# Optimization experiments

Hardware: AMD Instinct MI355X
Metric: run time of the kernel (lower is better)

The kernel has to match this reference:

```python
import jax, jax.numpy as jnp
import numpy as np
import math

B, T, C = 8, 1024, 64  # n_head = 1 (forced by the module's relative-attention matmul shapes)


def setup_inputs() -> dict:
    key = jax.random.key(0)
    ks = jax.random.split(key, 7)
    x = jax.random.normal(ks[0], (B, T, C), dtype=jnp.float32)
    Wqkv = jax.random.normal(ks[1], (3 * C, C), dtype=jnp.float32) * 0.02
    bqkv = jnp.zeros((3 * C,), dtype=jnp.float32)
    embk = jax.random.normal(ks[2], (T, C), dtype=jnp.float32) * 0.02
    embv = jax.random.normal(ks[3], (T, C), dtype=jnp.float32) * 0.02
    Wproj = jax.random.normal(ks[4], (C, C), dtype=jnp.float32) * 0.02
    bproj = jnp.zeros((C,), dtype=jnp.float32)
    return {"x": x, "Wqkv": Wqkv, "bqkv": bqkv, "embk": embk, "embv": embv,
            "Wproj": Wproj, "bproj": bproj}


def reference(x, Wqkv, bqkv, embk, embv, Wproj, bproj):
    b, t, c = x.shape
    qkv = x @ Wqkv.T + bqkv                      # [B,T,3C]
    q, k, v = jnp.split(qkv, 3, axis=2)          # each [B,T,C]; n_head=1 so head_dim=C

    # relative_pos[i,j] = (i-j).tril() -> 0 above diagonal (masked out anyway)
    idx = jnp.arange(t)
    rel = jnp.tril(idx[:, None] - idx[None, :])  # [T,T] ints in [0, T-1]
    rk = embk[rel]                               # [T,T,C] gathered relative keys
    rv = embv[rel]                               # [T,T,C] gathered relative values

    att1 = jnp.einsum('btc,bsc->bts', q, k)      # content-content scores
    att2 = jnp.einsum('tbc,tsc->bts', q.transpose(1, 0, 2), rk)  # content-position scores
    scale = 1.0 / math.sqrt(c)
    att = (att1 + att2) * scale

    causal = jnp.tril(jnp.ones((t, t), dtype=bool))
    att = jnp.where(causal[None, :, :], att, -jnp.inf)
    att = jax.nn.softmax(att, axis=-1)           # [B,T,T]

    y1 = jnp.einsum('bts,bsc->btc', att, v)      # content values
    y2 = jnp.einsum('bts,tsc->btc', att, rv)     # relative values
    y = y1 + y2                                  # [B,T,C]
    return y @ Wproj.T + bproj
```

## Files before the change

### kernel.cpp

```cpp
#include <hip/hip_runtime.h>
#include <math.h>

#define BB 8
#define TT 1024
#define CC 64

typedef float f32x4 __attribute__((ext_vector_type(4)));
typedef short short8 __attribute__((ext_vector_type(8)));
typedef unsigned int u32x4 __attribute__((ext_vector_type(4)));
typedef unsigned short u16;

static __device__ __forceinline__ u16 f2bf(float f) {
    union { float f; unsigned int u; } v; v.f = f;
    unsigned int r = v.u + 0x7fffu + ((v.u >> 16) & 1u);
    return (u16)(r >> 16);
}
static __device__ __forceinline__ float bf2f(u16 h) {
    union { unsigned int u; float f; } v; v.u = ((unsigned int)h) << 16; return v.f;
}
static __device__ __forceinline__ short8 pack8(const float* p) {
    float4 a = *(const float4*)p;
    float4 b = *(const float4*)(p + 4);
    short8 r;
    r[0] = (short)f2bf(a.x); r[1] = (short)f2bf(a.y); r[2] = (short)f2bf(a.z); r[3] = (short)f2bf(a.w);
    r[4] = (short)f2bf(b.x); r[5] = (short)f2bf(b.y); r[6] = (short)f2bf(b.z); r[7] = (short)f2bf(b.w);
    return r;
}

#define MFMA16(a, b, c) __builtin_amdgcn_mfma_f32_16x16x32_bf16((a), (b), (c), 0, 0, 0)

#define OFF_QBF      ((size_t)0)
#define OFF_KBF      ((size_t)1048576)
#define OFF_VT       ((size_t)2097152)
#define OFF_EKP      ((size_t)3145728)
#define OFF_EVT      ((size_t)3284992)
#define OFF_WPROJ    ((size_t)3424256)
#define OFF_YP       ((size_t)3432448)
#define OFF_LP       ((size_t)20209664)
#define WS_NEED      ((size_t)20471808)

__global__ __launch_bounds__(256) void qkv_prep_kernel(const float* __restrict__ x,
                                                       const float* __restrict__ Wqkv,
                                                       const float* __restrict__ bqkv,
                                                       const float* __restrict__ embk,
                                                       const float* __restrict__ embv,
                                                       const float* __restrict__ Wproj,
                                                       u16* __restrict__ q_bf,
                                                       u16* __restrict__ k_bf,
                                                       u16* __restrict__ vT_bf,
                                                       u16* __restrict__ embk_pad,
                                                       u16* __restrict__ embvT_pad,
                                                       u16* __restrict__ Wproj_bf) {
    const int blk = blockIdx.x;
    const int grp = blockIdx.y;
    const int tid = threadIdx.x;

    if (blk >= 512) {
        if (grp != 0) return;
        const int idx0 = (blk - 512) * 256 + tid;
        const int stride = 64 * 256;
        for (int i = idx0; i < 1088 * CC; i += stride) {
            int r = i >> 6, c = i & 63, d = r - 32;
            embk_pad[i] = (d >= 0 && d < TT) ? f2bf(embk[d * CC + c]) : (u16)0;
        }
        for (int i = idx0; i < CC * 1088; i += stride) {
            int c = i / 1088, col = i - c * 1088, d = col - 32;
            embvT_pad[i] = (d >= 0 && d < TT) ? f2bf(embv[d * CC + c]) : (u16)0;
        }
        for (int i = idx0; i < CC * CC; i += stride) Wproj_bf[i] = f2bf(Wproj[i]);
        return;
    }

    const int w = tid >> 6, lane = tid & 63, quad = lane >> 4, l15 = lane & 15;
    const int row0 = blk * 16;
    const int oc = grp * 4 + w;
    __shared__ float vt[4][16][17];

    const float* xr = x + (size_t)(row0 + l15) * CC + quad * 8;
    short8 a0 = pack8(xr);
    short8 a1 = pack8(xr + 32);

    const float* wr = Wqkv + (size_t)(oc * 16 + l15) * CC + quad * 8;
    short8 b0 = pack8(wr);
    short8 b1 = pack8(wr + 32);
    f32x4 acc = {0.f, 0.f, 0.f, 0.f};
    acc = MFMA16(a0, b0, acc);
    acc = MFMA16(a1, b1, acc);
    const float bias = bqkv[oc * 16 + l15];

    if (oc < 4) {
        const int c = oc * 16 + l15;
        #pragma unroll
        for (int r = 0; r < 4; ++r)
            q_bf[(size_t)(row0 + quad * 4 + r) * CC + c] = f2bf((acc[r] + bias) * 0.125f);
    } else if (oc < 8) {
        const int c = (oc - 4) * 16 + l15;
        #pragma unroll
        for (int r = 0; r < 4; ++r)
            k_bf[(size_t)(row0 + quad * 4 + r) * CC + c] = f2bf(acc[r] + bias);
    } else {
        #pragma unroll
        for (int r = 0; r < 4; ++r) vt[w][quad * 4 + r][l15] = acc[r] + bias;
        const int c_l = lane >> 2;
        const int tbase = (lane & 3) * 4;
        const int b = row0 >> 10, t0v = row0 & (TT - 1);
        u16 p[4];
        #pragma unroll
        for (int tt2 = 0; tt2 < 4; ++tt2) p[tt2] = f2bf(vt[w][tbase + tt2][c_l]);
        unsigned long long pk = (unsigned long long)p[0] | ((unsigned long long)p[1] << 16)
                              | ((unsigned long long)p[2] << 32) | ((unsigned long long)p[3] << 48);
        *(unsigned long long*)&vT_bf[(size_t)(b * CC + (oc - 8) * 16 + c_l) * TT + t0v + tbase] = pk;
    }
}

#define WBSTRIDE 4160

__global__ __launch_bounds__(256) void attn_part_kernel(const u16* __restrict__ q_bf,
                                                        const u16* __restrict__ k_bf,
                                                        const u16* __restrict__ vT_bf,
                                                        const u16* __restrict__ embk_pad,
                                                        const u16* __restrict__ embvT_pad,
                                                        float* __restrict__ Ypart,
                                                        float* __restrict__ Lpart) {
    const int b = blockIdx.y;
    int xx = blockIdx.x;
    int tt = 0, slot = 0;
    for (tt = 0; tt < 64; ++tt) {
        const int c = ((tt >> 1) + 4) >> 2;
        if (xx < c) { slot = xx; break; }
        xx -= c;
    }
    const int t0 = tt * 16;
    const int nst = (t0 >> 5) + 1;

    const int tid = threadIdx.x;
    const int w = tid >> 6, lane = tid & 63, quad = lane >> 4, l15 = lane & 15;
    const int st = slot * 4 + w;
    const bool active = (st < nst);

    __shared__ __align__(16) char wbuf[4][WBSTRIDE];
    __shared__ float lpart[4][16];

    u16* pt = (u16*)(wbuf[w]);
    u16* a2 = (u16*)(wbuf[w] + 1280);

    f32x4 acc[4];
    #pragma unroll
    for (int nb = 0; nb < 4; ++nb) acc[nb] = (f32x4){0.f, 0.f, 0.f, 0.f};
    float rsum[4] = {0.f, 0.f, 0.f, 0.f};

    if (active) {
        const int s0 = st * 32;

        const u16* qrow = q_bf + (size_t)((b << 10) + t0 + l15) * CC;
        short8 aq0 = *(const short8*)(qrow + quad * 8);
        short8 aq1 = *(const short8*)(qrow + 32 + quad * 8);

        f32x4 sc[2];
        #pragma unroll
        for (int cb = 0; cb < 2; ++cb) {
            const u16* krow = k_bf + (size_t)((b << 10) + s0 + cb * 16 + l15) * CC;
            short8 kb0 = *(const short8*)(krow + quad * 8);
            short8 kb1 = *(const short8*)(krow + 32 + quad * 8);
            f32x4 a = {0.f, 0.f, 0.f, 0.f};
            a = MFMA16(aq0, kb0, a);
            a = MFMA16(aq1, kb1, a);
            sc[cb] = a;
        }

        const int dbase = t0 - s0 - 31;
        f32x4 bnd[3];
        #pragma unroll
        for (int nb = 0; nb < 3; ++nb) {
            const u16* erow = embk_pad + (size_t)(dbase + 32 + nb * 16 + l15) * CC;
            short8 eb0 = *(const short8*)(erow + quad * 8);
            short8 eb1 = *(const short8*)(erow + 32 + quad * 8);
            f32x4 a = {0.f, 0.f, 0.f, 0.f};
            a = MFMA16(aq0, eb0, a);
            a = MFMA16(aq1, eb1, a);
            bnd[nb] = a;
        }

        u16 pb0[4], pb1[4];
        #pragma unroll
        for (int r = 0; r < 4; ++r) {
            const int i = quad * 4 + r;
            const int u0 = 31 + i - l15;
            const int src = (quad << 4) | (u0 & 15);
            const float v0 = __shfl(bnd[0][r], src, 64);
            const float v1 = __shfl(bnd[1][r], src, 64);
            const float v2 = __shfl(bnd[2][r], src, 64);
            const bool hi = (u0 >= 32);
            {
                const float rb = hi ? v2 : v1;
                const int d = t0 - s0 + i - l15;
                float pv = (d >= 0) ? __expf(sc[0][r] + rb) : 0.f;
                pb0[r] = f2bf(pv);
                rsum[r] += bf2f(pb0[r]);
            }
            {
                const float rb = hi ? v1 : v0;
                const int d = t0 - s0 + i - 16 - l15;
                float pv = (d >= 0) ? __expf(sc[1][r] + rb) : 0.f;
                pb1[r] = f2bf(pv);
                rsum[r] += bf2f(pb1[r]);
            }
        }

        u32x4 z = {0u, 0u, 0u, 0u};
        #pragma unroll
        for (int e = 0; e < 3; ++e) {
            int idx = lane + e * 64;
            if (idx < 144) ((u32x4*)a2)[idx] = z;
        }
        #pragma unroll
        for (int r = 0; r < 4; ++r) {
            const int i = quad * 4 + r;
            pt[i * 40 + l15] = pb0[r];
            pt[i * 40 + 16 + l15] = pb1[r];
            a2[i * 72 + (32 + i - l15)] = pb0[r];
            a2[i * 72 + (16 + i - l15)] = pb1[r];
        }

        short8 aP = *(const short8*)(pt + l15 * 40 + quad * 8);
        #pragma unroll
        for (int nb = 0; nb < 4; ++nb) {
            const u16* vrow = vT_bf + ((size_t)(b * CC + nb * 16 + l15) << 10) + s0;
            short8 bv = *(const short8*)(vrow + quad * 8);
            acc[nb] = MFMA16(aP, bv, acc[nb]);
        }

        const int dcol0 = t0 - s0;
        #pragma unroll
        for (int kk = 0; kk < 2; ++kk) {
            short8 a2f = *(const short8*)(a2 + l15 * 72 + kk * 32 + quad * 8);
            #pragma unroll
            for (int nb = 0; nb < 4; ++nb) {
                const u16* erow = embvT_pad + (size_t)(nb * 16 + l15) * 1088 + dcol0 + kk * 32 + quad * 8;
                short8 be = *(const short8*)erow;
                acc[nb] = MFMA16(a2f, be, acc[nb]);
            }
        }
    }

    #pragma unroll
    for (int msk = 1; msk < 16; msk <<= 1)
        #pragma unroll
        for (int r = 0; r < 4; ++r) rsum[r] += __shfl_xor(rsum[r], msk, 64);
    if (l15 == 0) {
        #pragma unroll
        for (int r = 0; r < 4; ++r) lpart[w][quad * 4 + r] = rsum[r];
    }

    float* ypw = (float*)(wbuf[w]);
    #pragma unroll
    for (int nb = 0; nb < 4; ++nb)
        #pragma unroll
        for (int r = 0; r < 4; ++r)
            ypw[(quad * 4 + r) * 64 + nb * 16 + l15] = acc[nb][r];
    __syncthreads();

    const size_t sbase = ((size_t)((b * 64 + tt) * 8 + slot)) << 10;
    {
        const int i = tid >> 4, c0 = (tid * 4) & 63;
        float4 Y;
        Y.x = ((float*)(wbuf[0]))[i * 64 + c0]     + ((float*)(wbuf[1]))[i * 64 + c0]
            + ((float*)(wbuf[2]))[i * 64 + c0]     + ((float*)(wbuf[3]))[i * 64 + c0];
        Y.y = ((float*)(wbuf[0]))[i * 64 + c0 + 1] + ((float*)(wbuf[1]))[i * 64 + c0 + 1]
            + ((float*)(wbuf[2]))[i * 64 + c0 + 1] + ((float*)(wbuf[3]))[i * 64 + c0 + 1];
        Y.z = ((float*)(wbuf[0]))[i * 64 + c0 + 2] + ((float*)(wbuf[1]))[i * 64 + c0 + 2]
            + ((float*)(wbuf[2]))[i * 64 + c0 + 2] + ((float*)(wbuf[3]))[i * 64 + c0 + 2];
        Y.w = ((float*)(wbuf[0]))[i * 64 + c0 + 3] + ((float*)(wbuf[1]))[i * 64 + c0 + 3]
            + ((float*)(wbuf[2]))[i * 64 + c0 + 3] + ((float*)(wbuf[3]))[i * 64 + c0 + 3];
        *(float4*)&Ypart[sbase + (size_t)tid * 4] = Y;
    }
    if (tid < 16)
        Lpart[((size_t)((b * 64 + tt) * 8 + slot)) * 16 + tid] =
            lpart[0][tid] + lpart[1][tid] + lpart[2][tid] + lpart[3][tid];
}

__global__ __launch_bounds__(256) void norm_proj_kernel(const float* __restrict__ Ypart,
                                                        const float* __restrict__ Lpart,
                                                        const u16* __restrict__ Wproj_bf,
                                                        const float* __restrict__ bproj,
                                                        float* __restrict__ out) {
    const int b = blockIdx.y;
    const int tt = blockIdx.x;
    const int t0 = tt * 16;
    const int nslots = ((tt >> 1) + 4) >> 2;
    const int tid = threadIdx.x;
    const int w = tid >> 6, lane = tid & 63, quad = lane >> 4, l15 = lane & 15;

    __shared__ float Ls[16];
    __shared__ __align__(16) u16 yA[16 * 64];

    const size_t base = ((size_t)((b * 64 + tt) * 8)) << 10;
    float4 Y = {0.f, 0.f, 0.f, 0.f};
    for (int s = 0; s < nslots; ++s) {
        float4 v = *(const float4*)&Ypart[base + ((size_t)s << 10) + (size_t)tid * 4];
        Y.x += v.x; Y.y += v.y; Y.z += v.z; Y.w += v.w;
    }
    if (tid < 16) {
        float L = 0.f;
        for (int s = 0; s < nslots; ++s)
            L += Lpart[((size_t)((b * 64 + tt) * 8 + s)) * 16 + tid];
        Ls[tid] = L;
    }
    __syncthreads();

    const int i = tid >> 4, c0 = (tid * 4) & 63;
    const float inv = 1.0f / Ls[i];
    u16 y4[4] = { f2bf(Y.x * inv), f2bf(Y.y * inv), f2bf(Y.z * inv), f2bf(Y.w * inv) };
    *(unsigned long long*)&yA[i * 64 + c0] =
        (unsigned long long)y4[0] | ((unsigned long long)y4[1] << 16)
      | ((unsigned long long)y4[2] << 32) | ((unsigned long long)y4[3] << 48);
    __syncthreads();

    short8 a0 = *(const short8*)(yA + l15 * 64 + quad * 8);
    short8 a1 = *(const short8*)(yA + l15 * 64 + 32 + quad * 8);
    const u16* wrow = Wproj_bf + (size_t)(w * 16 + l15) * CC;
    short8 wb0 = *(const short8*)(wrow + quad * 8);
    short8 wb1 = *(const short8*)(wrow + 32 + quad * 8);
    f32x4 o = {0.f, 0.f, 0.f, 0.f};
    o = MFMA16(a0, wb0, o);
    o = MFMA16(a1, wb1, o);
    const float bias = bproj[w * 16 + l15];
    #pragma unroll
    for (int r = 0; r < 4; ++r)
        out[(size_t)((b << 10) + t0 + quad * 4 + r) * CC + w * 16 + l15] = o[r] + bias;
}

__global__ __launch_bounds__(192) void qkv_kernel(const float* __restrict__ x,
                                                  const float* __restrict__ Wqkv,
                                                  const float* __restrict__ bqkv,
                                                  float* __restrict__ qkv) {
    __shared__ __align__(16) float xs[CC];
    const int row = blockIdx.x;
    const int j = threadIdx.x;
    if (j < CC) xs[j] = x[row * CC + j];
    __syncthreads();
    const float* w = Wqkv + j * CC;
    float acc = bqkv[j];
    #pragma unroll
    for (int c = 0; c < CC; c += 4) {
        float4 wq = *(const float4*)(w + c);
        float4 xq = *(const float4*)(xs + c);
        acc += wq.x * xq.x + wq.y * xq.y + wq.z * xq.z + wq.w * xq.w;
    }
    qkv[row * 192 + j] = acc;
}

__global__ __launch_bounds__(256) void attn_kernel(const float* __restrict__ qkv,
                                                   const float* __restrict__ embk,
                                                   const float* __restrict__ embv,
                                                   const float* __restrict__ Wproj,
                                                   const float* __restrict__ bproj,
                                                   float* __restrict__ out) {
    __shared__ __align__(16) float qs[CC];
    __shared__ __align__(16) float sc[TT];
    __shared__ float red[256];
    __shared__ float yred[4][CC];
    const int bt = blockIdx.x;
    const int b = bt >> 10, t = bt & (TT - 1);
    const int tid = threadIdx.x;
    if (tid < CC) qs[tid] = qkv[bt * 192 + tid];
    __syncthreads();
    float lmax = -1e30f;
    for (int s = tid; s <= t; s += 256) {
        const float* krow = qkv + (b * TT + s) * 192 + 64;
        const float* erow = embk + (t - s) * CC;
        float acc = 0.f;
        #pragma unroll
        for (int c = 0; c < CC; c += 4) {
            float4 kq = *(const float4*)(krow + c);
            float4 eq = *(const float4*)(erow + c);
            float4 qq = *(const float4*)(qs + c);
            acc += qq.x * (kq.x + eq.x) + qq.y * (kq.y + eq.y)
                 + qq.z * (kq.z + eq.z) + qq.w * (kq.w + eq.w);
        }
        acc *= 0.125f;
        sc[s] = acc;
        lmax = fmaxf(lmax, acc);
    }
    red[tid] = lmax; __syncthreads();
    for (int off = 128; off > 0; off >>= 1) { if (tid < off) red[tid] = fmaxf(red[tid], red[tid + off]); __syncthreads(); }
    const float m = red[0]; __syncthreads();
    float lsum = 0.f;
    for (int s = tid; s <= t; s += 256) { float e = __expf(sc[s] - m); sc[s] = e; lsum += e; }
    red[tid] = lsum; __syncthreads();
    for (int off = 128; off > 0; off >>= 1) { if (tid < off) red[tid] += red[tid + off]; __syncthreads(); }
    const float inv = 1.0f / red[0]; __syncthreads();
    const int c = tid & 63, g = tid >> 6;
    float acc = 0.f;
    for (int s = g; s <= t; s += 4) {
        float p = sc[s];
        float vv = qkv[(b * TT + s) * 192 + 128 + c];
        float ev = embv[(t - s) * CC + c];
        acc += p * (vv + ev);
    }
    yred[g][c] = acc * inv;
    __syncthreads();
    if (tid < CC) qs[tid] = yred[0][tid] + yred[1][tid] + yred[2][tid] + yred[3][tid];
    __syncthreads();
    if (tid < CC) {
        const float* w = Wproj + tid * CC;
        float o = bproj[tid];
        #pragma unroll
        for (int cc2 = 0; cc2 < CC; cc2 += 4) {
            float4 wq = *(const float4*)(w + cc2);
            float4 yq = *(const float4*)(qs + cc2);
            o += wq.x * yq.x + wq.y * yq.y + wq.z * yq.z + wq.w * yq.w;
        }
        out[bt * CC + tid] = o;
    }
}

extern "C" void kernel_launch(void* const* d_in, const int* in_sizes, int n_in,
                              void* d_out, int out_size, void* d_ws, size_t ws_size,
                              hipStream_t stream) {
    const float* x     = (const float*)d_in[0];
    const float* Wqkv  = (const float*)d_in[1];
    const float* bqkv  = (const float*)d_in[2];
    const float* embk  = (const float*)d_in[3];
    const float* embv  = (const float*)d_in[4];
    const float* Wproj = (const float*)d_in[5];
    const float* bproj = (const float*)d_in[6];
    float* out = (float*)d_out;

    if (ws_size < WS_NEED) {
        float* qkv = (float*)d_ws;
        qkv_kernel<<<BB * TT, 192, 0, stream>>>(x, Wqkv, bqkv, qkv);
        attn_kernel<<<BB * TT, 256, 0, stream>>>(qkv, embk, embv, Wproj, bproj, out);
        return;
    }

    char* ws = (char*)d_ws;
    u16* q_bf       = (u16*)(ws + OFF_QBF);
    u16* k_bf       = (u16*)(ws + OFF_KBF);
    u16* vT_bf      = (u16*)(ws + OFF_VT);
    u16* embk_pad   = (u16*)(ws + OFF_EKP);
    u16* embvT_pad  = (u16*)(ws + OFF_EVT);
    u16* Wproj_bf   = (u16*)(ws + OFF_WPROJ);
    float* Ypart    = (float*)(ws + OFF_YP);
    float* Lpart    = (float*)(ws + OFF_LP);

    qkv_prep_kernel<<<dim3(576, 3), 256, 0, stream>>>(x, Wqkv, bqkv, embk, embv, Wproj,
                                                      q_bf, k_bf, vT_bf, embk_pad, embvT_pad, Wproj_bf);
    attn_part_kernel<<<dim3(288, 8), 256, 0, stream>>>(q_bf, k_bf, vT_bf, embk_pad, embvT_pad,
                                                       Ypart, Lpart);
    norm_proj_kernel<<<dim3(64, 8), 256, 0, stream>>>(Ypart, Lpart, Wproj_bf, bproj, out);
}
```

Measured before the change: 110.6 us.

## Fuse split-K reduction and projection into attention kernel via atomic ticket

New measurement: 333.0 us. 3.01x slower.

```diff
diff --git a/kernel.cpp b/kernel.cpp
--- a/kernel.cpp
+++ b/kernel.cpp
@@ -37,7 +37,8 @@
 #define OFF_WPROJ    ((size_t)3424256)
 #define OFF_YP       ((size_t)3432448)
 #define OFF_LP       ((size_t)20209664)
-#define WS_NEED      ((size_t)20471808)
+#define OFF_CNT      ((size_t)20471808)
+#define WS_NEED      ((size_t)20473856)
 
 __global__ __launch_bounds__(256) void qkv_prep_kernel(const float* __restrict__ x,
                                                        const float* __restrict__ Wqkv,
@@ -120,8 +121,12 @@
                                                         const u16* __restrict__ vT_bf,
                                                         const u16* __restrict__ embk_pad,
                                                         const u16* __restrict__ embvT_pad,
+                                                        const u16* __restrict__ Wproj_bf,
+                                                        const float* __restrict__ bproj,
                                                         float* __restrict__ Ypart,
-                                                        float* __restrict__ Lpart) {
+                                                        float* __restrict__ Lpart,
+                                                        int* __restrict__ cnt,
+                                                        float* __restrict__ out) {
     const int b = blockIdx.y;
     int xx = blockIdx.x;
     int tt = 0, slot = 0;
@@ -132,6 +137,7 @@
     }
     const int t0 = tt * 16;
     const int nst = (t0 >> 5) + 1;
+    const int nslots = ((tt >> 1) + 4) >> 2;
 
     const int tid = threadIdx.x;
     const int w = tid >> 6, lane = tid & 63, quad = lane >> 4, l15 = lane & 15;
@@ -140,6 +146,7 @@
 
     __shared__ __align__(16) char wbuf[4][WBSTRIDE];
     __shared__ float lpart[4][16];
+    __shared__ int ticket_s;
 
     u16* pt = (u16*)(wbuf[w]);
     u16* a2 = (u16*)(wbuf[w] + 1280);
@@ -260,39 +267,32 @@
             ypw[(quad * 4 + r) * 64 + nb * 16 + l15] = acc[nb][r];
     __syncthreads();
 
+    const int i4 = tid >> 4, c04 = (tid * 4) & 63;
     const size_t sbase = ((size_t)((b * 64 + tt) * 8 + slot)) << 10;
     {
-        const int i = tid >> 4, c0 = (tid * 4) & 63;
         float4 Y;
-        Y.x = ((float*)(wbuf[0]))[i * 64 + c0]     + ((float*)(wbuf[1]))[i * 64 + c0]
-            + ((float*)(wbuf[2]))[i * 64 + c0]     + ((float*)(wbuf[3]))[i * 64 + c0];
-        Y.y = ((float*)(wbuf[0]))[i * 64 + c0 + 1] + ((float*)(wbuf[1]))[i * 64 + c0 + 1]
-            + ((float*)(wbuf[2]))[i * 64 + c0 + 1] + ((float*)(wbuf[3]))[i * 64 + c0 + 1];
-        Y.z = ((float*)(wbuf[0]))[i * 64 + c0 + 2] + ((float*)(wbuf[1]))[i * 64 + c0 + 2]
-            + ((float*)(wbuf[2]))[i * 64 + c0 + 2] + ((float*)(wbuf[3]))[i * 64 + c0 + 2];
-        Y.w = ((float*)(wbuf[0]))[i * 64 + c0 + 3] + ((float*)(wbuf[1]))[i * 64 + c0 + 3]
-            + ((float*)(wbuf[2]))[i * 64 + c0 + 3] + ((float*)(wbuf[3]))[i * 64 + c0 + 3];
+        Y.x = ((float*)(wbuf[0]))[i4 * 64 + c04]     + ((float*)(wbuf[1]))[i4 * 64 + c04]
+            + ((float*)(wbuf[2]))[i4 * 64 + c04]     + ((float*)(wbuf[3]))[i4 * 64 + c04];
+        Y.y = ((float*)(wbuf[0]))[i4 * 64 + c04 + 1] + ((float*)(wbuf[1]))[i4 * 64 + c04 + 1]
+            + ((float*)(wbuf[2]))[i4 * 64 + c04 + 1] + ((float*)(wbuf[3]))[i4 * 64 + c04 + 1];
+        Y.z = ((float*)(wbuf[0]))[i4 * 64 + c04 + 2] + ((float*)(wbuf[1]))[i4 * 64 + c04 + 2]
+            + ((float*)(wbuf[2]))[i4 * 64 + c04 + 2] + ((float*)(wbuf[3]))[i4 * 64 + c04 + 2];
+        Y.w = ((float*)(wbuf[0]))[i4 * 64 + c04 + 3] + ((float*)(wbuf[1]))[i4 * 64 + c04 + 3]
+            + ((float*)(wbuf[2]))[i4 * 64 + c04 + 3] + ((float*)(wbuf[3]))[i4 * 64 + c04 + 3];
         *(float4*)&Ypart[sbase + (size_t)tid * 4] = Y;
     }
     if (tid < 16)
         Lpart[((size_t)((b * 64 + tt) * 8 + slot)) * 16 + tid] =
             lpart[0][tid] + lpart[1][tid] + lpart[2][tid] + lpart[3][tid];
-}
-
-__global__ __launch_bounds__(256) void norm_proj_kernel(const float* __restrict__ Ypart,
-                                                        const float* __restrict__ Lpart,
-                                                        const u16* __restrict__ Wproj_bf,
-                                                        const float* __restrict__ bproj,
-                                                        float* __restrict__ out) {
-    const int b = blockIdx.y;
-    const int tt = blockIdx.x;
-    const int t0 = tt * 16;
-    const int nslots = ((tt >> 1) + 4) >> 2;
-    const int tid = threadIdx.x;
-    const int w = tid >> 6, lane = tid & 63, quad = lane >> 4, l15 = lane & 15;
-
-    __shared__ float Ls[16];
-    __shared__ __align__(16) u16 yA[16 * 64];
+    __syncthreads();
+
+    if (tid == 0) {
+        __threadfence();
+        ticket_s = atomicAdd(&cnt[b * 64 + tt], 1);
+    }
+    __syncthreads();
+    if (ticket_s != nslots - 1) return;
+    __threadfence();
 
     const size_t base = ((size_t)((b * 64 + tt) * 8)) << 10;
     float4 Y = {0.f, 0.f, 0.f, 0.f};
@@ -300,6 +300,7 @@
         float4 v = *(const float4*)&Ypart[base + ((size_t)s << 10) + (size_t)tid * 4];
         Y.x += v.x; Y.y += v.y; Y.z += v.z; Y.w += v.w;
     }
+    float* Ls = lpart[0];
     if (tid < 16) {
         float L = 0.f;
         for (int s = 0; s < nslots; ++s)
@@ -308,12 +309,14 @@
     }
     __syncthreads();
 
-    const int i = tid >> 4, c0 = (tid * 4) & 63;
-    const float inv = 1.0f / Ls[i];
-    u16 y4[4] = { f2bf(Y.x * inv), f2bf(Y.y * inv), f2bf(Y.z * inv), f2bf(Y.w * inv) };
-    *(unsigned long long*)&yA[i * 64 + c0] =
-        (unsigned long long)y4[0] | ((unsigned long long)y4[1] << 16)
-      | ((unsigned long long)y4[2] << 32) | ((unsigned long long)y4[3] << 48);
+    u16* yA = (u16*)(wbuf[1]);
+    {
+        const float inv = 1.0f / Ls[i4];
+        u16 y4[4] = { f2bf(Y.x * inv), f2bf(Y.y * inv), f2bf(Y.z * inv), f2bf(Y.w * inv) };
+        *(unsigned long long*)&yA[i4 * 64 + c04] =
+            (unsigned long long)y4[0] | ((unsigned long long)y4[1] << 16)
+          | ((unsigned long long)y4[2] << 32) | ((unsigned long long)y4[3] << 48);
+    }
     __syncthreads();
 
     short8 a0 = *(const short8*)(yA + l15 * 64 + quad * 8);
@@ -443,10 +446,11 @@
     u16* Wproj_bf   = (u16*)(ws + OFF_WPROJ);
     float* Ypart    = (float*)(ws + OFF_YP);
     float* Lpart    = (float*)(ws + OFF_LP);
-
+    int*   cnt      = (int*)(ws + OFF_CNT);
+
+    hipMemsetAsync(cnt, 0, 8 * 64 * sizeof(int), stream);
     qkv_prep_kernel<<<dim3(576, 3), 256, 0, stream>>>(x, Wqkv, bqkv, embk, embv, Wproj,
                                                       q_bf, k_bf, vT_bf, embk_pad, embvT_pad, Wproj_bf);
     attn_part_kernel<<<dim3(288, 8), 256, 0, stream>>>(q_bf, k_bf, vT_bf, embk_pad, embvT_pad,
-                                                       Ypart, Lpart);
-    norm_proj_kernel<<<dim3(64, 8), 256, 0, stream>>>(Ypart, Lpart, Wproj_bf, bproj, out);
-}
+                                                       Wproj_bf, bproj, Ypart, Lpart, cnt, out);
+}
```

## Split attention into one-wave blocks per key tile, drop in-block reduction

Applied to the files above, without the earlier changes.

Measured after the change: 124.0 us. 12.1% more time.

```diff
diff --git a/kernel.cpp b/kernel.cpp
--- a/kernel.cpp
+++ b/kernel.cpp
@@ -36,8 +36,9 @@
 #define OFF_EVT      ((size_t)3284992)
 #define OFF_WPROJ    ((size_t)3424256)
 #define OFF_YP       ((size_t)3432448)
-#define OFF_LP       ((size_t)20209664)
-#define WS_NEED      ((size_t)20471808)
+#define OFF_LP       ((size_t)38035456)
+#define WS_NEED      ((size_t)38576128)
+
 
 __global__ __launch_bounds__(256) void qkv_prep_kernel(const float* __restrict__ x,
                                                        const float* __restrict__ Wqkv,
@@ -113,133 +114,122 @@
     }
 }
 
-#define WBSTRIDE 4160
-
-__global__ __launch_bounds__(256) void attn_part_kernel(const u16* __restrict__ q_bf,
-                                                        const u16* __restrict__ k_bf,
-                                                        const u16* __restrict__ vT_bf,
-                                                        const u16* __restrict__ embk_pad,
-                                                        const u16* __restrict__ embvT_pad,
-                                                        float* __restrict__ Ypart,
-                                                        float* __restrict__ Lpart) {
+__global__ __launch_bounds__(64) void attn_part_kernel(const u16* __restrict__ q_bf,
+                                                       const u16* __restrict__ k_bf,
+                                                       const u16* __restrict__ vT_bf,
+                                                       const u16* __restrict__ embk_pad,
+                                                       const u16* __restrict__ embvT_pad,
+                                                       float* __restrict__ Ypart,
+                                                       float* __restrict__ Lpart) {
     const int b = blockIdx.y;
     int xx = blockIdx.x;
-    int tt = 0, slot = 0;
+    int tt = 0, st = 0;
     for (tt = 0; tt < 64; ++tt) {
-        const int c = ((tt >> 1) + 4) >> 2;
-        if (xx < c) { slot = xx; break; }
+        const int c = (tt >> 1) + 1;
+        if (xx < c) { st = xx; break; }
         xx -= c;
     }
     const int t0 = tt * 16;
-    const int nst = (t0 >> 5) + 1;
-
-    const int tid = threadIdx.x;
-    const int w = tid >> 6, lane = tid & 63, quad = lane >> 4, l15 = lane & 15;
-    const int st = slot * 4 + w;
-    const bool active = (st < nst);
-
-    __shared__ __align__(16) char wbuf[4][WBSTRIDE];
-    __shared__ float lpart[4][16];
-
-    u16* pt = (u16*)(wbuf[w]);
-    u16* a2 = (u16*)(wbuf[w] + 1280);
+    const int s0 = st * 32;
+
+    const int lane = threadIdx.x, quad = lane >> 4, l15 = lane & 15;
+
+    __shared__ __align__(16) char wbuf[4160];
+    u16* pt = (u16*)(wbuf);
+    u16* a2 = (u16*)(wbuf + 1280);
 
     f32x4 acc[4];
     #pragma unroll
     for (int nb = 0; nb < 4; ++nb) acc[nb] = (f32x4){0.f, 0.f, 0.f, 0.f};
     float rsum[4] = {0.f, 0.f, 0.f, 0.f};
 
-    if (active) {
-        const int s0 = st * 32;
-
-        const u16* qrow = q_bf + (size_t)((b << 10) + t0 + l15) * CC;
-        short8 aq0 = *(const short8*)(qrow + quad * 8);
-        short8 aq1 = *(const short8*)(qrow + 32 + quad * 8);
-
-        f32x4 sc[2];
-        #pragma unroll
-        for (int cb = 0; cb < 2; ++cb) {
-            const u16* krow = k_bf + (size_t)((b << 10) + s0 + cb * 16 + l15) * CC;
-            short8 kb0 = *(const short8*)(krow + quad * 8);
-            short8 kb1 = *(const short8*)(krow + 32 + quad * 8);
-            f32x4 a = {0.f, 0.f, 0.f, 0.f};
-            a = MFMA16(aq0, kb0, a);
-            a = MFMA16(aq1, kb1, a);
-            sc[cb] = a;
-        }
-
-        const int dbase = t0 - s0 - 31;
-        f32x4 bnd[3];
-        #pragma unroll
-        for (int nb = 0; nb < 3; ++nb) {
-            const u16* erow = embk_pad + (size_t)(dbase + 32 + nb * 16 + l15) * CC;
-            short8 eb0 = *(const short8*)(erow + quad * 8);
-            short8 eb1 = *(const short8*)(erow + 32 + quad * 8);
-            f32x4 a = {0.f, 0.f, 0.f, 0.f};
-            a = MFMA16(aq0, eb0, a);
-            a = MFMA16(aq1, eb1, a);
-            bnd[nb] = a;
-        }
-
-        u16 pb0[4], pb1[4];
-        #pragma unroll
-        for (int r = 0; r < 4; ++r) {
-            const int i = quad * 4 + r;
-            const int u0 = 31 + i - l15;
-            const int src = (quad << 4) | (u0 & 15);
-            const float v0 = __shfl(bnd[0][r], src, 64);
-            const float v1 = __shfl(bnd[1][r], src, 64);
-            const float v2 = __shfl(bnd[2][r], src, 64);
-            const bool hi = (u0 >= 32);
-            {
-                const float rb = hi ? v2 : v1;
-                const int d = t0 - s0 + i - l15;
-                float pv = (d >= 0) ? __expf(sc[0][r] + rb) : 0.f;
-                pb0[r] = f2bf(pv);
-                rsum[r] += bf2f(pb0[r]);
-            }
-            {
-                const float rb = hi ? v1 : v0;
-                const int d = t0 - s0 + i - 16 - l15;
-                float pv = (d >= 0) ? __expf(sc[1][r] + rb) : 0.f;
-                pb1[r] = f2bf(pv);
-                rsum[r] += bf2f(pb1[r]);
-            }
-        }
-
-        u32x4 z = {0u, 0u, 0u, 0u};
-        #pragma unroll
-        for (int e = 0; e < 3; ++e) {
-            int idx = lane + e * 64;
-            if (idx < 144) ((u32x4*)a2)[idx] = z;
-        }
-        #pragma unroll
-        for (int r = 0; r < 4; ++r) {
-            const int i = quad * 4 + r;
-            pt[i * 40 + l15] = pb0[r];
-            pt[i * 40 + 16 + l15] = pb1[r];
-            a2[i * 72 + (32 + i - l15)] = pb0[r];
-            a2[i * 72 + (16 + i - l15)] = pb1[r];
-        }
-
-        short8 aP = *(const short8*)(pt + l15 * 40 + quad * 8);
+    const u16* qrow = q_bf + (size_t)((b << 10) + t0 + l15) * CC;
+    short8 aq0 = *(const short8*)(qrow + quad * 8);
+    short8 aq1 = *(const short8*)(qrow + 32 + quad * 8);
+
+    f32x4 sc[2];
+    #pragma unroll
+    for (int cb = 0; cb < 2; ++cb) {
+        const u16* krow = k_bf + (size_t)((b << 10) + s0 + cb * 16 + l15) * CC;
+        short8 kb0 = *(const short8*)(krow + quad * 8);
+        short8 kb1 = *(const short8*)(krow + 32 + quad * 8);
+        f32x4 a = {0.f, 0.f, 0.f, 0.f};
+        a = MFMA16(aq0, kb0, a);
+        a = MFMA16(aq1, kb1, a);
+        sc[cb] = a;
+    }
+
+    const int dbase = t0 - s0 - 31;
+    f32x4 bnd[3];
+    #pragma unroll
+    for (int nb = 0; nb < 3; ++nb) {
+        const u16* erow = embk_pad + (size_t)(dbase + 32 + nb * 16 + l15) * CC;
+        short8 eb0 = *(const short8*)(erow + quad * 8);
+        short8 eb1 = *(const short8*)(erow + 32 + quad * 8);
+        f32x4 a = {0.f, 0.f, 0.f, 0.f};
+        a = MFMA16(aq0, eb0, a);
+        a = MFMA16(aq1, eb1, a);
+        bnd[nb] = a;
+    }
+
+    u16 pb0[4], pb1[4];
+    #pragma unroll
+    for (int r = 0; r < 4; ++r) {
+        const int i = quad * 4 + r;
+        const int u0 = 31 + i - l15;
+        const int src = (quad << 4) | (u0 & 15);
+        const float v0 = __shfl(bnd[0][r], src, 64);
+        const float v1 = __shfl(bnd[1][r], src, 64);
+        const float v2 = __shfl(bnd[2][r], src, 64);
+        const bool hi = (u0 >= 32);
+        {
+            const float rb = hi ? v2 : v1;
+            const int d = t0 - s0 + i - l15;
+            float pv = (d >= 0) ? __expf(sc[0][r] + rb) : 0.f;
+            pb0[r] = f2bf(pv);
+            rsum[r] += bf2f(pb0[r]);
+        }
+        {
+            const float rb = hi ? v1 : v0;
+            const int d = t0 - s0 + i - 16 - l15;
+            float pv = (d >= 0) ? __expf(sc[1][r] + rb) : 0.f;
+            pb1[r] = f2bf(pv);
+            rsum[r] += bf2f(pb1[r]);
+        }
+    }
+
+    u32x4 z = {0u, 0u, 0u, 0u};
+    #pragma unroll
+    for (int e = 0; e < 3; ++e) {
+        int idx = lane + e * 64;
+        if (idx < 144) ((u32x4*)a2)[idx] = z;
+    }
+    #pragma unroll
+    for (int r = 0; r < 4; ++r) {
+        const int i = quad * 4 + r;
+        pt[i * 40 + l15] = pb0[r];
+        pt[i * 40 + 16 + l15] = pb1[r];
+        a2[i * 72 + (32 + i - l15)] = pb0[r];
+        a2[i * 72 + (16 + i - l15)] = pb1[r];
+    }
+
+    short8 aP = *(const short8*)(pt + l15 * 40 + quad * 8);
+    #pragma unroll
+    for (int nb = 0; nb < 4; ++nb) {
+        const u16* vrow = vT_bf + ((size_t)(b * CC + nb * 16 + l15) << 10) + s0;
+        short8 bv = *(const short8*)(vrow + quad * 8);
+        acc[nb] = MFMA16(aP, bv, acc[nb]);
+    }
+
+    const int dcol0 = t0 - s0;
+    #pragma unroll
+    for (int kk = 0; kk < 2; ++kk) {
+        short8 a2f = *(const short8*)(a2 + l15 * 72 + kk * 32 + quad * 8);
         #pragma unroll
         for (int nb = 0; nb < 4; ++nb) {
-            const u16* vrow = vT_bf + ((size_t)(b * CC + nb * 16 + l15) << 10) + s0;
-            short8 bv = *(const short8*)(vrow + quad * 8);
-            acc[nb] = MFMA16(aP, bv, acc[nb]);
-        }
-
-        const int dcol0 = t0 - s0;
-        #pragma unroll
-        for (int kk = 0; kk < 2; ++kk) {
-            short8 a2f = *(const short8*)(a2 + l15 * 72 + kk * 32 + quad * 8);
-            #pragma unroll
-            for (int nb = 0; nb < 4; ++nb) {
-                const u16* erow = embvT_pad + (size_t)(nb * 16 + l15) * 1088 + dcol0 + kk * 32 + quad * 8;
-                short8 be = *(const short8*)erow;
-                acc[nb] = MFMA16(a2f, be, acc[nb]);
-            }
+            const u16* erow = embvT_pad + (size_t)(nb * 16 + l15) * 1088 + dcol0 + kk * 32 + quad * 8;
+            short8 be = *(const short8*)erow;
+            acc[nb] = MFMA16(a2f, be, acc[nb]);
         }
     }
 
@@ -247,36 +237,24 @@
     for (int msk = 1; msk < 16; msk <<= 1)
         #pragma unroll
         for (int r = 0; r < 4; ++r) rsum[r] += __shfl_xor(rsum[r], msk, 64);
+    const size_t pslot = (size_t)(b * 1056 + blockIdx.x);
     if (l15 == 0) {
         #pragma unroll
-        for (int r = 0; r < 4; ++r) lpart[w][quad * 4 + r] = rsum[r];
-    }
-
-    float* ypw = (float*)(wbuf[w]);
+        for (int r = 0; r < 4; ++r) Lpart[pslot * 16 + quad * 4 + r] = rsum[r];
+    }
+
+    float* ypw = (float*)(wbuf);
     #pragma unroll
     for (int nb = 0; nb < 4; ++nb)
         #pragma unroll
         for (int r = 0; r < 4; ++r)
             ypw[(quad * 4 + r) * 64 + nb * 16 + l15] = acc[nb][r];
-    __syncthreads();
-
-    const size_t sbase = ((size_t)((b * 64 + tt) * 8 + slot)) << 10;
-    {
-        const int i = tid >> 4, c0 = (tid * 4) & 63;
-        float4 Y;
-        Y.x = ((float*)(wbuf[0]))[i * 64 + c0]     + ((float*)(wbuf[1]))[i * 64 + c0]
-            + ((float*)(wbuf[2]))[i * 64 + c0]     + ((float*)(wbuf[3]))[i * 64 + c0];
-        Y.y = ((float*)(wbuf[0]))[i * 64 + c0 + 1] + ((float*)(wbuf[1]))[i * 64 + c0 + 1]
-            + ((float*)(wbuf[2]))[i * 64 + c0 + 1] + ((float*)(wbuf[3]))[i * 64 + c0 + 1];
-        Y.z = ((float*)(wbuf[0]))[i * 64 + c0 + 2] + ((float*)(wbuf[1]))[i * 64 + c0 + 2]
-            + ((float*)(wbuf[2]))[i * 64 + c0 + 2] + ((float*)(wbuf[3]))[i * 64 + c0 + 2];
-        Y.w = ((float*)(wbuf[0]))[i * 64 + c0 + 3] + ((float*)(wbuf[1]))[i * 64 + c0 + 3]
-            + ((float*)(wbuf[2]))[i * 64 + c0 + 3] + ((float*)(wbuf[3]))[i * 64 + c0 + 3];
-        *(float4*)&Ypart[sbase + (size_t)tid * 4] = Y;
-    }
-    if (tid < 16)
-        Lpart[((size_t)((b * 64 + tt) * 8 + slot)) * 16 + tid] =
-            lpart[0][tid] + lpart[1][tid] + lpart[2][tid] + lpart[3][tid];
+    const size_t sbase = pslot << 10;
+    #pragma unroll
+    for (int k2 = 0; k2 < 4; ++k2) {
+        float4 v = *(const float4*)&ypw[(lane + k2 * 64) * 4];
+        *(float4*)&Ypart[sbase + (size_t)(lane + k2 * 64) * 4] = v;
+    }
 }
 
 __global__ __launch_bounds__(256) void norm_proj_kernel(const float* __restrict__ Ypart,
@@ -287,23 +265,25 @@
     const int b = blockIdx.y;
     const int tt = blockIdx.x;
     const int t0 = tt * 16;
-    const int nslots = ((tt >> 1) + 4) >> 2;
+    const int nst = (tt >> 1) + 1;
+    const int h = tt >> 1;
+    const int sbegin = (tt & 1) ? (h + 1) * (h + 1) : h * (h + 1);
     const int tid = threadIdx.x;
     const int w = tid >> 6, lane = tid & 63, quad = lane >> 4, l15 = lane & 15;
 
     __shared__ float Ls[16];
     __shared__ __align__(16) u16 yA[16 * 64];
 
-    const size_t base = ((size_t)((b * 64 + tt) * 8)) << 10;
+    const size_t base = ((size_t)(b * 1056 + sbegin)) << 10;
     float4 Y = {0.f, 0.f, 0.f, 0.f};
-    for (int s = 0; s < nslots; ++s) {
+    for (int s = 0; s < nst; ++s) {
         float4 v = *(const float4*)&Ypart[base + ((size_t)s << 10) + (size_t)tid * 4];
         Y.x += v.x; Y.y += v.y; Y.z += v.z; Y.w += v.w;
     }
     if (tid < 16) {
         float L = 0.f;
-        for (int s = 0; s < nslots; ++s)
-            L += Lpart[((size_t)((b * 64 + tt) * 8 + s)) * 16 + tid];
+        for (int s = 0; s < nst; ++s)
+            L += Lpart[(size_t)(b * 1056 + sbegin + s) * 16 + tid];
         Ls[tid] = L;
     }
     __syncthreads();
@@ -446,7 +426,7 @@
 
     qkv_prep_kernel<<<dim3(576, 3), 256, 0, stream>>>(x, Wqkv, bqkv, embk, embv, Wproj,
                                                       q_bf, k_bf, vT_bf, embk_pad, embvT_pad, Wproj_bf);
-    attn_part_kernel<<<dim3(288, 8), 256, 0, stream>>>(q_bf, k_bf, vT_bf, embk_pad, embvT_pad,
+    attn_part_kernel<<<dim3(1056, 8), 64, 0, stream>>>(q_bf, k_bf, vT_bf, embk_pad, embvT_pad,
                                                        Ypart, Lpart);
     norm_proj_kernel<<<dim3(64, 8), 256, 0, stream>>>(Ypart, Lpart, Wproj_bf, bproj, out);
 }
```

## Process two key tiles per warp and compact partial-sum buffers

Applied to the files above, without the earlier changes.

After: 113.5 us. 2.6% more time.

```diff
diff --git a/kernel.cpp b/kernel.cpp
--- a/kernel.cpp
+++ b/kernel.cpp
@@ -36,8 +36,8 @@
 #define OFF_EVT      ((size_t)3284992)
 #define OFF_WPROJ    ((size_t)3424256)
 #define OFF_YP       ((size_t)3432448)
-#define OFF_LP       ((size_t)20209664)
-#define WS_NEED      ((size_t)20471808)
+#define OFF_LP       ((size_t)8675328)
+#define WS_NEED      ((size_t)8757248)
 
 __global__ __launch_bounds__(256) void qkv_prep_kernel(const float* __restrict__ x,
                                                        const float* __restrict__ Wqkv,
@@ -113,7 +113,103 @@
     }
 }
 
-#define WBSTRIDE 4160
+static __device__ __forceinline__ void process_tile(int b, int t0, int s0,
+                                                    int lane, int quad, int l15,
+                                                    short8 aq0, short8 aq1,
+                                                    const u16* __restrict__ k_bf,
+                                                    const u16* __restrict__ embk_pad,
+                                                    const u16* __restrict__ vT_bf,
+                                                    const u16* __restrict__ embvT_pad,
+                                                    u16* pt, u16* a2,
+                                                    f32x4 acc[4], float rsum[4]) {
+    f32x4 sc[2];
+    #pragma unroll
+    for (int cb = 0; cb < 2; ++cb) {
+        const u16* krow = k_bf + (size_t)((b << 10) + s0 + cb * 16 + l15) * CC;
+        short8 kb0 = *(const short8*)(krow + quad * 8);
+        short8 kb1 = *(const short8*)(krow + 32 + quad * 8);
+        f32x4 a = {0.f, 0.f, 0.f, 0.f};
+        a = MFMA16(aq0, kb0, a);
+        a = MFMA16(aq1, kb1, a);
+        sc[cb] = a;
+    }
+
+    const int dbase = t0 - s0 - 31;
+    f32x4 bnd[3];
+    #pragma unroll
+    for (int nb = 0; nb < 3; ++nb) {
+        const u16* erow = embk_pad + (size_t)(dbase + 32 + nb * 16 + l15) * CC;
+        short8 eb0 = *(const short8*)(erow + quad * 8);
+        short8 eb1 = *(const short8*)(erow + 32 + quad * 8);
+        f32x4 a = {0.f, 0.f, 0.f, 0.f};
+        a = MFMA16(aq0, eb0, a);
+        a = MFMA16(aq1, eb1, a);
+        bnd[nb] = a;
+    }
+
+    u16 pb0[4], pb1[4];
+    #pragma unroll
+    for (int r = 0; r < 4; ++r) {
+        const int i = quad * 4 + r;
+        const int u0 = 31 + i - l15;
+        const int src = (quad << 4) | (u0 & 15);
+        const float v0 = __shfl(bnd[0][r], src, 64);
+        const float v1 = __shfl(bnd[1][r], src, 64);
+        const float v2 = __shfl(bnd[2][r], src, 64);
+        const bool hi = (u0 >= 32);
+        {
+            const float rb = hi ? v2 : v1;
+            const int d = t0 - s0 + i - l15;
+            float pv = (d >= 0) ? __expf(sc[0][r] + rb) : 0.f;
+            pb0[r] = f2bf(pv);
+            rsum[r] += bf2f(pb0[r]);
+        }
+        {
+            const float rb = hi ? v1 : v0;
+            const int d = t0 - s0 + i - 16 - l15;
+            float pv = (d >= 0) ? __expf(sc[1][r] + rb) : 0.f;
+            pb1[r] = f2bf(pv);
+            rsum[r] += bf2f(pb1[r]);
+        }
+    }
+
+    u32x4 z = {0u, 0u, 0u, 0u};
+    #pragma unroll
+    for (int e = 0; e < 3; ++e) {
+        int idx = lane + e * 64;
+        if (idx < 144) ((u32x4*)a2)[idx] = z;
+    }
+    #pragma unroll
+    for (int r = 0; r < 4; ++r) {
+        const int i = quad * 4 + r;
+        pt[i * 40 + l15] = pb0[r];
+        pt[i * 40 + 16 + l15] = pb1[r];
+        a2[i * 72 + (32 + i - l15)] = pb0[r];
+        a2[i * 72 + (16 + i - l15)] = pb1[r];
+    }
+
+    short8 aP = *(const short8*)(pt + l15 * 40 + quad * 8);
+    #pragma unroll
+    for (int nb = 0; nb < 4; ++nb) {
+        const u16* vrow = vT_bf + ((size_t)(b * CC + nb * 16 + l15) << 10) + s0;
+        short8 bv = *(const short8*)(vrow + quad * 8);
+        acc[nb] = MFMA16(aP, bv, acc[nb]);
+    }
+
+    const int dcol0 = t0 - s0;
+    #pragma unroll
+    for (int kk = 0; kk < 2; ++kk) {
+        short8 a2f = *(const short8*)(a2 + l15 * 72 + kk * 32 + quad * 8);
+        #pragma unroll
+        for (int nb = 0; nb < 4; ++nb) {
+            const u16* erow = embvT_pad + (size_t)(nb * 16 + l15) * 1088 + dcol0 + kk * 32 + quad * 8;
+            short8 be = *(const short8*)erow;
+            acc[nb] = MFMA16(a2f, be, acc[nb]);
+        }
+    }
+}
+
+#define WBSTRIDE 7168
 
 __global__ __launch_bounds__(256) void attn_part_kernel(const u16* __restrict__ q_bf,
                                                         const u16* __restrict__ k_bf,
@@ -126,122 +222,38 @@
     int xx = blockIdx.x;
     int tt = 0, slot = 0;
     for (tt = 0; tt < 64; ++tt) {
-        const int c = ((tt >> 1) + 4) >> 2;
+        const int c = ((tt >> 1) + 8) >> 3;
         if (xx < c) { slot = xx; break; }
         xx -= c;
     }
     const int t0 = tt * 16;
-    const int nst = (t0 >> 5) + 1;
+    const int nst = (tt >> 1) + 1;
 
     const int tid = threadIdx.x;
     const int w = tid >> 6, lane = tid & 63, quad = lane >> 4, l15 = lane & 15;
-    const int st = slot * 4 + w;
-    const bool active = (st < nst);
+    const int stA = slot * 8 + w;
+    const int stB = slot * 8 + 4 + w;
 
     __shared__ __align__(16) char wbuf[4][WBSTRIDE];
     __shared__ float lpart[4][16];
 
-    u16* pt = (u16*)(wbuf[w]);
-    u16* a2 = (u16*)(wbuf[w] + 1280);
-
     f32x4 acc[4];
     #pragma unroll
     for (int nb = 0; nb < 4; ++nb) acc[nb] = (f32x4){0.f, 0.f, 0.f, 0.f};
     float rsum[4] = {0.f, 0.f, 0.f, 0.f};
 
-    if (active) {
-        const int s0 = st * 32;
-
-        const u16* qrow = q_bf + (size_t)((b << 10) + t0 + l15) * CC;
-        short8 aq0 = *(const short8*)(qrow + quad * 8);
-        short8 aq1 = *(const short8*)(qrow + 32 + quad * 8);
-
-        f32x4 sc[2];
-        #pragma unroll
-        for (int cb = 0; cb < 2; ++cb) {
-            const u16* krow = k_bf + (size_t)((b << 10) + s0 + cb * 16 + l15) * CC;
-            short8 kb0 = *(const short8*)(krow + quad * 8);
-            short8 kb1 = *(const short8*)(krow + 32 + quad * 8);
-            f32x4 a = {0.f, 0.f, 0.f, 0.f};
-            a = MFMA16(aq0, kb0, a);
-            a = MFMA16(aq1, kb1, a);
-            sc[cb] = a;
-        }
-
-        const int dbase = t0 - s0 - 31;
-        f32x4 bnd[3];
-        #pragma unroll
-        for (int nb = 0; nb < 3; ++nb) {
-            const u16* erow = embk_pad + (size_t)(dbase + 32 + nb * 16 + l15) * CC;
-            short8 eb0 = *(const short8*)(erow + quad * 8);
-            short8 eb1 = *(const short8*)(erow + 32 + quad * 8);
-            f32x4 a = {0.f, 0.f, 0.f, 0.f};
-            a = MFMA16(aq0, eb0, a);
-            a = MFMA16(aq1, eb1, a);
-            bnd[nb] = a;
-        }
-
-        u16 pb0[4], pb1[4];
-        #pragma unroll
-        for (int r = 0; r < 4; ++r) {
-            const int i = quad * 4 + r;
-            const int u0 = 31 + i - l15;
-            const int src = (quad << 4) | (u0 & 15);
-            const float v0 = __shfl(bnd[0][r], src, 64);
-            const float v1 = __shfl(bnd[1][r], src, 64);
-            const float v2 = __shfl(bnd[2][r], src, 64);
-            const bool hi = (u0 >= 32);
-            {
-                const float rb = hi ? v2 : v1;
-                const int d = t0 - s0 + i - l15;
-                float pv = (d >= 0) ? __expf(sc[0][r] + rb) : 0.f;
-                pb0[r] = f2bf(pv);
-                rsum[r] += bf2f(pb0[r]);
-            }
-            {
-                const float rb = hi ? v1 : v0;
-                const int d = t0 - s0 + i - 16 - l15;
-                float pv = (d >= 0) ? __expf(sc[1][r] + rb) : 0.f;
-                pb1[r] = f2bf(pv);
-                rsum[r] += bf2f(pb1[r]);
-            }
-        }
-
-        u32x4 z = {0u, 0u, 0u, 0u};
-        #pragma unroll
-        for (int e = 0; e < 3; ++e) {
-            int idx = lane + e * 64;
-            if (idx < 144) ((u32x4*)a2)[idx] = z;
-        }
-        #pragma unroll
-        for (int r = 0; r < 4; ++r) {
-            const int i = quad * 4 + r;
-            pt[i * 40 + l15] = pb0[r];
-            pt[i * 40 + 16 + l15] = pb1[r];
-            a2[i * 72 + (32 + i - l15)] = pb0[r];
-            a2[i * 72 + (16 + i - l15)] = pb1[r];
-        }
-
-        short8 aP = *(const short8*)(pt + l15 * 40 + quad * 8);
-        #pragma unroll
-        for (int nb = 0; nb < 4; ++nb) {
-            const u16* vrow = vT_bf + ((size_t)(b * CC + nb * 16 + l15) << 10) + s0;
-            short8 bv = *(const short8*)(vrow + quad * 8);
-            acc[nb] = MFMA16(aP, bv, acc[nb]);
-        }
-
-        const int dcol0 = t0 - s0;
-        #pragma unroll
-        for (int kk = 0; kk < 2; ++kk) {
-            short8 a2f = *(const short8*)(a2 + l15 * 72 + kk * 32 + quad * 8);
-            #pragma unroll
-            for (int nb = 0; nb < 4; ++nb) {
-                const u16* erow = embvT_pad + (size_t)(nb * 16 + l15) * 1088 + dcol0 + kk * 32 + quad * 8;
-                short8 be = *(const short8*)erow;
-                acc[nb] = MFMA16(a2f, be, acc[nb]);
-            }
-        }
-    }
+    const u16* qrow = q_bf + (size_t)((b << 10) + t0 + l15) * CC;
+    short8 aq0 = *(const short8*)(qrow + quad * 8);
+    short8 aq1 = *(const short8*)(qrow + 32 + quad * 8);
+
+    if (stA < nst)
+        process_tile(b, t0, stA * 32, lane, quad, l15, aq0, aq1,
+                     k_bf, embk_pad, vT_bf, embvT_pad,
+                     (u16*)(wbuf[w]), (u16*)(wbuf[w] + 1280), acc, rsum);
+    if (stB < nst)
+        process_tile(b, t0, stB * 32, lane, quad, l15, aq0, aq1,
+                     k_bf, embk_pad, vT_bf, embvT_pad,
+                     (u16*)(wbuf[w] + 3584), (u16*)(wbuf[w] + 4864), acc, rsum);
 
     #pragma unroll
     for (int msk = 1; msk < 16; msk <<= 1)
@@ -260,23 +272,22 @@
             ypw[(quad * 4 + r) * 64 + nb * 16 + l15] = acc[nb][r];
     __syncthreads();
 
-    const size_t sbase = ((size_t)((b * 64 + tt) * 8 + slot)) << 10;
+    const int i4 = tid >> 4, c04 = (tid * 4) & 63;
+    const size_t pslot = (size_t)(b * 160 + blockIdx.x);
     {
-        const int i = tid >> 4, c0 = (tid * 4) & 63;
         float4 Y;
-        Y.x = ((float*)(wbuf[0]))[i * 64 + c0]     + ((float*)(wbuf[1]))[i * 64 + c0]
-            + ((float*)(wbuf[2]))[i * 64 + c0]     + ((float*)(wbuf[3]))[i * 64 + c0];
-        Y.y = ((float*)(wbuf[0]))[i * 64 + c0 + 1] + ((float*)(wbuf[1]))[i * 64 + c0 + 1]
-            + ((float*)(wbuf[2]))[i * 64 + c0 + 1] + ((float*)(wbuf[3]))[i * 64 + c0 + 1];
-        Y.z = ((float*)(wbuf[0]))[i * 64 + c0 + 2] + ((float*)(wbuf[1]))[i * 64 + c0 + 2]
-            + ((float*)(wbuf[2]))[i * 64 + c0 + 2] + ((float*)(wbuf[3]))[i * 64 + c0 + 2];
-        Y.w = ((float*)(wbuf[0]))[i * 64 + c0 + 3] + ((float*)(wbuf[1]))[i * 64 + c0 + 3]
-            + ((float*)(wbuf[2]))[i * 64 + c0 + 3] + ((float*)(wbuf[3]))[i * 64 + c0 + 3];
-        *(float4*)&Ypart[sbase + (size_t)tid * 4] = Y;
+        Y.x = ((float*)(wbuf[0]))[i4 * 64 + c04]     + ((float*)(wbuf[1]))[i4 * 64 + c04]
+            + ((float*)(wbuf[2]))[i4 * 64 + c04]     + ((float*)(wbuf[3]))[i4 * 64 + c04];
+        Y.y = ((float*)(wbuf[0]))[i4 * 64 + c04 + 1] + ((float*)(wbuf[1]))[i4 * 64 + c04 + 1]
+            + ((float*)(wbuf[2]))[i4 * 64 + c04 + 1] + ((float*)(wbuf[3]))[i4 * 64 + c04 + 1];
+        Y.z = ((float*)(wbuf[0]))[i4 * 64 + c04 + 2] + ((float*)(wbuf[1]))[i4 * 64 + c04 + 2]
+            + ((float*)(wbuf[2]))[i4 * 64 + c04 + 2] + ((float*)(wbuf[3]))[i4 * 64 + c04 + 2];
+        Y.w = ((float*)(wbuf[0]))[i4 * 64 + c04 + 3] + ((float*)(wbuf[1]))[i4 * 64 + c04 + 3]
+            + ((float*)(wbuf[2]))[i4 * 64 + c04 + 3] + ((float*)(wbuf[3]))[i4 * 64 + c04 + 3];
+        *(float4*)&Ypart[(pslot << 10) + (size_t)tid * 4] = Y;
     }
     if (tid < 16)
-        Lpart[((size_t)((b * 64 + tt) * 8 + slot)) * 16 + tid] =
-            lpart[0][tid] + lpart[1][tid] + lpart[2][tid] + lpart[3][tid];
+        Lpart[pslot * 16 + tid] = lpart[0][tid] + lpart[1][tid] + lpart[2][tid] + lpart[3][tid];
 }
 
 __global__ __launch_bounds__(256) void norm_proj_kernel(const float* __restrict__ Ypart,
@@ -287,14 +298,16 @@
     const int b = blockIdx.y;
     const int tt = blockIdx.x;
     const int t0 = tt * 16;
-    const int nslots = ((tt >> 1) + 4) >> 2;
+    const int nslots = ((tt >> 1) + 8) >> 3;
+    int sbegin = 0;
+    for (int t2 = 0; t2 < tt; ++t2) sbegin += ((t2 >> 1) + 8) >> 3;
     const int tid = threadIdx.x;
     const int w = tid >> 6, lane = tid & 63, quad = lane >> 4, l15 = lane & 15;
 
     __shared__ float Ls[16];
     __shared__ __align__(16) u16 yA[16 * 64];
 
-    const size_t base = ((size_t)((b * 64 + tt) * 8)) << 10;
+    const size_t base = ((size_t)(b * 160 + sbegin)) << 10;
     float4 Y = {0.f, 0.f, 0.f, 0.f};
     for (int s = 0; s < nslots; ++s) {
         float4 v = *(const float4*)&Ypart[base + ((size_t)s << 10) + (size_t)tid * 4];
@@ -303,7 +316,7 @@
     if (tid < 16) {
         float L = 0.f;
         for (int s = 0; s < nslots; ++s)
-            L += Lpart[((size_t)((b * 64 + tt) * 8 + s)) * 16 + tid];
+            L += Lpart[(size_t)(b * 160 + sbegin + s) * 16 + tid];
         Ls[tid] = L;
     }
     __syncthreads();
@@ -446,7 +459,7 @@
 
     qkv_prep_kernel<<<dim3(576, 3), 256, 0, stream>>>(x, Wqkv, bqkv, embk, embv, Wproj,
                                                       q_bf, k_bf, vT_bf, embk_pad, embvT_pad, Wproj_bf);
-    attn_part_kernel<<<dim3(288, 8), 256, 0, stream>>>(q_bf, k_bf, vT_bf, embk_pad, embvT_pad,
+    attn_part_kernel<<<dim3(160, 8), 256, 0, stream>>>(q_bf, k_bf, vT_bf, embk_pad, embvT_pad,
                                                        Ypart, Lpart);
     norm_proj_kernel<<<dim3(64, 8), 256, 0, stream>>>(Ypart, Lpart, Wproj_bf, bproj, out);
 }
```
